# Performance work log

Measured on AMD Instinct MI355X. Metric: run time of the kernel, lower is better.

## Reference

```python
import jax, jax.numpy as jnp
import numpy as np

N, F, H, Z = 80, 64, 256, 128
OFF = N * (N - 1) // 2  # 3160
E = 800
MPM_ITERS = 50


def _gcn(x, src, dst, W, b, n):
    # PyG GCNConv: add self-loops, symmetric normalization D^-1/2 (A+I) D^-1/2, then +bias
    h = x @ W
    ones = jnp.ones(src.shape[0], dtype=h.dtype)
    deg = jax.ops.segment_sum(ones, dst, num_segments=n)
    dinv = jax.lax.rsqrt(jnp.maximum(deg, 1e-12))
    norm = dinv[src] * dinv[dst]
    out = jax.ops.segment_sum(h[src] * norm[:, None], dst, num_segments=n)
    return out + b


def _bn(h, g, b):
    # BatchNorm1d, training mode (biased batch stats), eps=1e-5
    m = h.mean(0)
    v = ((h - m) ** 2).mean(0)
    return g * (h - m) * jax.lax.rsqrt(v + 1e-5) + b


def setup_inputs() -> dict:
    key = jax.random.key(0)
    ks = jax.random.split(key, 32)
    rn = lambda k, s, sc=0.05: (jax.random.normal(k, s, dtype=jnp.float32) * sc)
    inp = {
        'x': jax.random.normal(ks[0], (N, F), dtype=jnp.float32),
        'edge_index': jax.random.randint(ks[1], (2, E), 0, N, dtype=jnp.int32),
        'adj': jax.random.randint(ks[2], (N, N), 0, 2, dtype=jnp.int32),
        'eps': jax.random.normal(ks[3], (1, Z), dtype=jnp.float32),
        'W1': rn(ks[4], (F, H)), 'b1': jnp.zeros((H,), jnp.float32),
        'g1': jnp.ones((H,), jnp.float32), 'bt1': jnp.zeros((H,), jnp.float32),
        'W2': rn(ks[5], (H, H)), 'b2': jnp.zeros((H,), jnp.float32),
        'g2': jnp.ones((H,), jnp.float32), 'bt2': jnp.zeros((H,), jnp.float32),
        'Wmu': rn(ks[6], (H, Z)), 'bmu': jnp.zeros((Z,), jnp.float32),
        'Wlv': rn(ks[7], (H, Z)), 'blv': jnp.zeros((Z,), jnp.float32),
        'We1': rn(ks[8], (Z, H)), 'be1': jnp.zeros((H,), jnp.float32),
        'We2': rn(ks[9], (H, OFF)), 'be2': jnp.zeros((OFF,), jnp.float32),
        'Wn1': rn(ks[10], (Z, H)), 'bn1': jnp.zeros((H,), jnp.float32),
        'Wn2': rn(ks[11], (H, N)), 'bn2': jnp.zeros((N,), jnp.float32),
    }
    return inp


def reference(x, edge_index, adj, eps, W1, b1, g1, bt1, W2, b2, g2, bt2,
              Wmu, bmu, Wlv, blv, We1, be1, We2, be2, Wn1, bn1, Wn2, bn2):
    n = N
    # ---- encoder: GCN -> BN -> ReLU (x2), mean pool over real nodes ----
    sl = jnp.arange(n, dtype=edge_index.dtype)
    src = jnp.concatenate([edge_index[0], sl])
    dst = jnp.concatenate([edge_index[1], sl])
    h = jax.nn.relu(_bn(_gcn(x, src, dst, W1, b1, n), g1, bt1))
    h = jax.nn.relu(_bn(_gcn(h, src, dst, W2, b2, n), g2, bt2))
    g_vec = h.sum(0, keepdims=True) / n  # [1,H], R_int == n
    mu = g_vec @ Wmu + bmu
    logvar = jnp.clip(g_vec @ Wlv + blv, -4.0, 4.0)
    z = mu + eps * jnp.exp(0.5 * logvar)  # reparam
    # ---- decoder ----
    vec_logits = (jax.nn.relu(z @ We1 + be1) @ We2 + be2)[0]   # [OFF]
    node_logits = (jax.nn.relu(z @ Wn1 + bn1) @ Wn2 + bn2)[0]  # [N]
    iu, ju = np.triu_indices(n, k=1)
    A_hat = jnp.zeros((n, n), jnp.float32).at[iu, ju].set(vec_logits)
    A_hat = A_hat + A_hat.T
    d = jnp.arange(n)
    A_hat = A_hat.at[d, d].set(node_logits)  # A_hat_logits
    # ---- edge similarity tensor S [N,N,N,N] ----
    A = jnp.maximum(adj, adj.T).astype(jnp.float32)
    A = A.at[d, d].set(1.0)
    B = jax.nn.sigmoid(A_hat).at[d, d].set(1.0)
    degA, degB = A.sum(1), B.sum(1)
    node_sim = 1.0 / (jnp.abs(degA[:, None] - degB[None, :]) + 1.0)
    dA, dB = jnp.diag(A), jnp.diag(B)  # all ones by construction (faithful to source)
    S = (A * dA[:, None] * dA[None, :])[:, :, None, None] * \
        (B * dB[:, None] * dB[None, :])[None, None, :, :]
    eye = jnp.eye(n, dtype=bool)
    xor = eye[:, :, None, None] ^ eye[None, None, :, :]
    S = jnp.where(xor, 0.0, S)
    both = eye[:, :, None, None] & eye[None, None, :, :]
    S = jnp.where(both, node_sim[:, None, :, None], S)
    # ---- MPM fixed point (fixed 50 iterations) ----
    notey = (~eye).astype(S.dtype)[:, :, None]  # [i,j,1]
    X0 = jnp.full((n, n), 1.0 / n, dtype=jnp.float32)

    def step(X, _):
        node_term = X * node_sim
        XS_max = jnp.max(S * X[None, :, None, :], axis=-1)  # [i,j,a] = max_b X[j,b]*S[i,j,a,b]
        edge_term = jnp.sum(XS_max * notey, axis=1)          # sum over j != i
        Xn = node_term + edge_term
        Xn = Xn / jnp.linalg.norm(Xn)
        return Xn, None

    X, _ = jax.lax.scan(step, X0, None, length=MPM_ITERS)
    return X
```

## Files before the change

### kernel.cpp

```cpp
#include <hip/hip_runtime.h>


#define NN 80
#define PBLK 20
#define TPB 320
#define RP 84
#define NCOLS 13

__device__ __forceinline__ float ld_f32g(const float* p){
  return __hip_atomic_load((float*)p, __ATOMIC_RELAXED, __HIP_MEMORY_SCOPE_AGENT);
}
__device__ __forceinline__ void st_f32g(float* p, float v){
  __hip_atomic_store(p, v, __ATOMIC_RELAXED, __HIP_MEMORY_SCOPE_AGENT);
}
__device__ __forceinline__ int ld_i32g(const int* p){
  return __hip_atomic_load((int*)p, __ATOMIC_RELAXED, __HIP_MEMORY_SCOPE_AGENT);
}
__device__ __forceinline__ void st_i32g(int* p, int v){
  __hip_atomic_store(p, v, __ATOMIC_RELAXED, __HIP_MEMORY_SCOPE_AGENT);
}
__device__ __forceinline__ float2 ld_f2g(const float* p){
  union { unsigned long long u; float2 f; } c;
  c.u = __hip_atomic_load((unsigned long long*)p, __ATOMIC_RELAXED, __HIP_MEMORY_SCOPE_AGENT);
  return c.f;
}
__device__ __forceinline__ void st_f2g(float* p, float a, float b){
  union { unsigned long long u; float2 f; } c; c.f.x = a; c.f.y = b;
  __hip_atomic_store((unsigned long long*)p, c.u, __ATOMIC_RELAXED, __HIP_MEMORY_SCOPE_AGENT);
}

__device__ __forceinline__ float wave_sum(float v){
  #pragma unroll
  for (int k = 32; k >= 1; k >>= 1) v += __shfl_xor(v, k, 64);
  return v;
}

__device__ void gcn_bn_relu(const float* inL, const float* bias, const float* gamma,
                            const float* beta, const int* ei, const float* dinvS,
                            float* accL, float* colstat, int p, int tid)
{
  for (int u = tid; u < NCOLS*NN; u += TPB) accL[u] = 0.f;
  __syncthreads();
  for (int cl = 0; cl < NCOLS; cl++){
    int c = p + PBLK*cl; if (c >= 256) break;
    const float* col = &inL[cl*NN];
    for (int e = tid; e < 800; e += TPB){
      int s = ei[e], d = ei[800+e];
      atomicAdd(&accL[cl*NN + d], col[s]*dinvS[s]*dinvS[d]);
    }
  }
  __syncthreads();
  for (int u = tid; u < NCOLS*NN; u += TPB){
    int cl = u/NN, i = u - cl*NN, c = p + PBLK*cl;
    if (c < 256) accL[u] += inL[u]*dinvS[i]*dinvS[i] + bias[c];
  }
  __syncthreads();
  if (tid < 16*NCOLS){
    int g = tid >> 4, s = tid & 15, c = p + PBLK*g;
    if (c < 256){
      float r[5];
      float sm = 0.f;
      #pragma unroll
      for (int i = 0; i < 5; i++){ r[i] = accL[g*NN + s + 16*i]; sm += r[i]; }
      #pragma unroll
      for (int k = 1; k < 16; k <<= 1) sm += __shfl_xor(sm, k, 64);
      float m = sm*(1.0f/NN);
      float sq = 0.f;
      #pragma unroll
      for (int i = 0; i < 5; i++){ float d = r[i]-m; sq += d*d; }
      #pragma unroll
      for (int k = 1; k < 16; k <<= 1) sq += __shfl_xor(sq, k, 64);
      if (s == 0){
        colstat[2*g]   = m;
        colstat[2*g+1] = 1.0f/sqrtf(sq*(1.0f/NN) + 1e-5f);
      }
    }
  }
  __syncthreads();
  for (int u = tid; u < NCOLS*NN; u += TPB){
    int cl = u/NN, c = p + PBLK*cl;
    if (c < 256){
      float hv = gamma[c]*(accL[u]-colstat[2*cl])*colstat[2*cl+1] + beta[c];
      accL[u] = fmaxf(hv, 0.f);
    }
  }
  __syncthreads();
}

__global__ __launch_bounds__(TPB, 1) void gvae_fused(
    const float* __restrict__ x,  const int* __restrict__ ei, const int* __restrict__ adj,
    const float* __restrict__ eps,
    const float* __restrict__ W1, const float* __restrict__ b1, const float* __restrict__ g1, const float* __restrict__ bt1,
    const float* __restrict__ W2, const float* __restrict__ b2, const float* __restrict__ g2, const float* __restrict__ bt2,
    const float* __restrict__ Wmu,const float* __restrict__ bmu,const float* __restrict__ Wlv,const float* __restrict__ blv,
    const float* __restrict__ We1,const float* __restrict__ be1,const float* __restrict__ We2,const float* __restrict__ be2,
    float* __restrict__ out, float* __restrict__ ws)
{
  const int tid = threadIdx.x;
  const int p   = blockIdx.x;

  int*   flag  = (int*)ws;
  float* slots = ws + 32;
  float* gvS   = ws + 1056;
  float* hT    = ws + 1312;
  float* Bm    = hT + 20480;
  float* Xb0   = Bm + 6400;
  float* Xb1   = Xb0 + 6400;

  __shared__ float Xs[NN*RP];
  __shared__ float MtL[4*RP];
  __shared__ float red[8];
  __shared__ float scS;
  __shared__ float dinvS[NN];
  __shared__ float accL[NCOLS*NN];
  __shared__ float hL[NCOLS*NN];
  __shared__ float gv[256], zv[128], t1v[256];
  __shared__ float colstat[2*NCOLS];

  for (int i = tid; i < NN; i += TPB) accL[i] = 1.0f;
  __syncthreads();
  for (int e = tid; e < 800; e += TPB) atomicAdd(&accL[ei[800+e]], 1.0f);
  __syncthreads();
  for (int i = tid; i < NN; i += TPB) dinvS[i] = 1.0f/sqrtf(accL[i]);
  __syncthreads();

  for (int u = tid; u < NCOLS*NN; u += TPB){
    int cl = u/NN, i = u - cl*NN, c = p + PBLK*cl;
    if (c < 256){
      float s = 0.f;
      for (int k = 0; k < 64; k++) s += x[i*64+k]*W1[k*256+c];
      hL[u] = s;
    }
  }
  __syncthreads();
  gcn_bn_relu(hL, b1, g1, bt1, ei, dinvS, accL, colstat, p, tid);
  for (int u2 = tid; u2 < 40*NCOLS; u2 += TPB){
    int cl = u2/40, i2 = (u2 - cl*40)*2, c = p + PBLK*cl;
    if (c < 256) st_f2g(&hT[c*NN+i2], accL[cl*NN+i2], accL[cl*NN+i2+1]);
  }
  __syncthreads();
  if (tid == 0) st_i32g(&flag[p], 1);

  if (tid < PBLK) while (ld_i32g(&flag[tid]) < 1) {}
  __syncthreads();
  for (int u = tid; u < 20*NCOLS; u += TPB){
    int cl = u/20, iq = u - cl*20, c = p + PBLK*cl;
    if (c < 256){
      int i0 = 4*iq;
      float a0=0.f,a1=0.f,a2=0.f,a3=0.f;
      for (int k = 0; k < 256; k++){
        float wv = W2[k*256+c];
        float2 h01 = ld_f2g(&hT[k*NN+i0]);
        float2 h23 = ld_f2g(&hT[k*NN+i0+2]);
        a0 += h01.x*wv; a1 += h01.y*wv; a2 += h23.x*wv; a3 += h23.y*wv;
      }
      hL[cl*NN+i0+0]=a0; hL[cl*NN+i0+1]=a1; hL[cl*NN+i0+2]=a2; hL[cl*NN+i0+3]=a3;
    }
  }
  __syncthreads();
  gcn_bn_relu(hL, b2, g2, bt2, ei, dinvS, accL, colstat, p, tid);
  if (tid < 16*NCOLS){
    int g = tid >> 4, s = tid & 15, c = p + PBLK*g;
    if (c < 256){
      float sm = 0.f;
      #pragma unroll
      for (int i = 0; i < 5; i++) sm += accL[g*NN + s + 16*i];
      #pragma unroll
      for (int k = 1; k < 16; k <<= 1) sm += __shfl_xor(sm, k, 64);
      if (s == 0) st_f32g(&gvS[c], sm*(1.0f/NN));
    }
  }
  __syncthreads();
  if (tid == 0) st_i32g(&flag[p], 2);

  if (tid < PBLK) while (ld_i32g(&flag[tid]) < 2) {}
  __syncthreads();
  if (tid < 256) gv[tid] = ld_f32g(&gvS[tid]);
  __syncthreads();
  if (tid < 128){
    int c = tid;
    float smu = bmu[c], slv = blv[c];
    for (int k = 0; k < 256; k++){
      float g = gv[k];
      smu += g*Wmu[k*128+c];
      slv += g*Wlv[k*128+c];
    }
    slv = fminf(fmaxf(slv, -4.f), 4.f);
    zv[c] = smu + eps[c]*expf(0.5f*slv);
  }
  __syncthreads();
  if (tid < 256){
    float s = be1[tid];
    for (int k = 0; k < 128; k++) s += zv[k]*We1[k*256+tid];
    t1v[tid] = fmaxf(s, 0.f);
  }
  __syncthreads();

  {
    int c0 = 79-p, c1 = 59-p, c2 = 39-p, c3 = 19-p;
    int t1b = c0+c1, t2b = t1b+c2, L = t2b+c3;
    int i = -1, j = -1;
    if      (tid < c0) { i = p;    j = p+1 +tid;        }
    else if (tid < t1b){ i = p+20; j = p+21+(tid-c0);   }
    else if (tid < t2b){ i = p+40; j = p+41+(tid-t1b);  }
    else if (tid < L)  { i = p+60; j = p+61+(tid-t2b);  }
    if (i >= 0){
      int off = i*(159-i)/2 + (j-i-1);
      float s = be2[off];
      for (int k = 0; k < 256; k++) s += t1v[k]*We2[k*3160+off];
      float sg = 1.0f/(1.0f + expf(-s));
      st_f32g(&Bm[i*NN+j], sg);
      st_f32g(&Bm[j*NN+i], sg);
    }
    if (tid >= 316){
      int r = tid-316, ii = p+20*r;
      st_f32g(&Bm[ii*NN+ii], 1.0f);
    }
  }
  __syncthreads();
  if (tid == 0) st_i32g(&flag[p], 3);

  const int w  = tid >> 6;
  const int l  = tid & 63;
  const int il = 16*w + (l & 15);
  const int ae = l >> 4;
  const int al = 4*p + ae;

  float4 Af[20];
  float degA = 0.f;
  #pragma unroll
  for (int c = 0; c < 20; c++){
    int j0 = 4*c;
    int4 ar = *(const int4*)&adj[il*NN+j0];
    int q0 = adj[(j0+0)*NN+il];
    int q1 = adj[(j0+1)*NN+il];
    int q2 = adj[(j0+2)*NN+il];
    int q3 = adj[(j0+3)*NN+il];
    float4 a;
    a.x = ((ar.x|q0) != 0 || il == j0+0) ? 1.f : 0.f;
    a.y = ((ar.y|q1) != 0 || il == j0+1) ? 1.f : 0.f;
    a.z = ((ar.z|q2) != 0 || il == j0+2) ? 1.f : 0.f;
    a.w = ((ar.w|q3) != 0 || il == j0+3) ? 1.f : 0.f;
    Af[c] = a;
    degA += (a.x+a.y)+(a.z+a.w);
  }

  if (tid < PBLK) while (ld_i32g(&flag[tid]) < 3) {}
  __syncthreads();

  float4 Bf[20];
  float degB = 0.f;
  #pragma unroll
  for (int c = 0; c < 20; c++){
    float2 b01 = ld_f2g(&Bm[al*NN+4*c]);
    float2 b23 = ld_f2g(&Bm[al*NN+4*c+2]);
    Bf[c].x = b01.x; Bf[c].y = b01.y; Bf[c].z = b23.x; Bf[c].w = b23.y;
    degB += (b01.x+b01.y)+(b23.x+b23.y);
  }
  const float ns = 1.0f/(fabsf(degA-degB)+1.0f);
  {
    if      (ae == 0) Bf[p].x = 0.f;
    else if (ae == 1) Bf[p].y = 0.f;
    else if (ae == 2) Bf[p].z = 0.f;
    else              Bf[p].w = 0.f;
  }

  for (int u = tid; u < NN*RP; u += TPB) Xs[u] = 1.0f/NN;
  __syncthreads();
  float xn = 0.f;
  for (int t = 0; t < 50; t++){
    float sc = 1.0f;
    if (t > 0){
      float pv = 0.f;
      if (tid < PBLK){
        const float* sp = &slots[(t-1)*PBLK + tid];
        do { pv = ld_f32g(sp); } while (pv == 0.0f);
      }
      if (w == 0){
        float v = pv;
        #pragma unroll
        for (int k = 1; k < 32; k <<= 1) v += __shfl_xor(v, k, 64);
        if (tid == 0) scS = 1.0f/sqrtf(v);
      }
      __syncthreads();
      sc = scS;
      const float* Xsrc = ((t-1)&1) ? Xb1 : Xb0;
      #pragma unroll
      for (int q = 0; q < 10; q++){
        int p2 = tid + TPB*q;
        int j = p2/40, c2 = p2 - 40*j;
        float2 xv = ld_f2g(&Xsrc[j*NN + 2*c2]);
        Xs[j*RP + 2*c2]     = xv.x;
        Xs[j*RP + 2*c2 + 1] = xv.y;
      }
      __syncthreads();
    }

    float m = 0.f;
    #pragma unroll
    for (int c = 0; c < 20; c++){
      float4 xv = *(const float4*)&Xs[il*RP+4*c];
      float p0 = xv.x*Bf[c].x, p1 = xv.y*Bf[c].y, p2 = xv.z*Bf[c].z, p3 = xv.w*Bf[c].w;
      m = fmaxf(m, fmaxf(fmaxf(p0,p1), fmaxf(p2,p3)));
    }
    float xnode = Xs[il*RP+al];
    MtL[ae*RP+il] = m;
    __syncthreads();

    float e0=0.f,e1=0.f,e2=0.f,e3=0.f;
    #pragma unroll
    for (int c = 0; c < 20; c++){
      float4 mv = *(const float4*)&MtL[ae*RP+4*c];
      e0 += Af[c].x*mv.x; e1 += Af[c].y*mv.y; e2 += Af[c].z*mv.z; e3 += Af[c].w*mv.w;
    }
    float edge = ((e0+e1)+(e2+e3)) - m;
    xn = sc*(ns*xnode + edge);

    if (t < 49){
      float* Xdst = (t&1) ? Xb1 : Xb0;
      st_f32g(&Xdst[il*NN+al], xn);
    }
    float v2 = wave_sum(xn*xn);
    if (l == 0) red[w] = v2;
    __syncthreads();
    if (tid == 0){
      float tot = ((red[0]+red[1])+(red[2]+red[3]))+red[4];
      st_f32g(&slots[t*PBLK+p], tot);
    }
  }

  {
    float pv = 0.f;
    if (tid < PBLK){
      const float* sp = &slots[49*PBLK + tid];
      do { pv = ld_f32g(sp); } while (pv == 0.0f);
    }
    if (w == 0){
      float v = pv;
      #pragma unroll
      for (int k = 1; k < 32; k <<= 1) v += __shfl_xor(v, k, 64);
      if (tid == 0) scS = 1.0f/sqrtf(v);
    }
    __syncthreads();
    out[il*NN+al] = xn * scS;
  }
}

extern "C" void kernel_launch(void* const* d_in, const int* in_sizes, int n_in,
                              void* d_out, int out_size, void* d_ws, size_t ws_size,
                              hipStream_t stream)
{
  (void)in_sizes; (void)n_in; (void)out_size; (void)ws_size;
  hipMemsetAsync(d_ws, 0, 4224, stream);
  gvae_fused<<<PBLK, TPB, 0, stream>>>(
      (const float*)d_in[0],  (const int*)d_in[1],   (const int*)d_in[2],   (const float*)d_in[3],
      (const float*)d_in[4],  (const float*)d_in[5],  (const float*)d_in[6],  (const float*)d_in[7],
      (const float*)d_in[8],  (const float*)d_in[9],  (const float*)d_in[10], (const float*)d_in[11],
      (const float*)d_in[12], (const float*)d_in[13], (const float*)d_in[14], (const float*)d_in[15],
      (const float*)d_in[16], (const float*)d_in[17], (const float*)d_in[18], (const float*)d_in[19],
      (float*)d_out, (float*)d_ws);
}
```

Measured before the change: 568.9 us.

## Compute decoder B rows locally, stage hT in LDS, coalesce X exchange stores

Each block now computes the four rows of the decoded sigmoid matrix it needs directly into shared memory. This removes the global Bm buffer and the grid-wide flag-3 barrier, at the cost of computing each off-diagonal entry twice across blocks. The second GCN matmul stages hT into LDS in 64-row chunks instead of reading global memory per thread. The MPM iteration stages outputs in LDS so they can be written as contiguous float2 per block, and the read side transposes into Xs. That adds one extra __syncthreads per iteration.

New measurement: 612.0 us. 7.6% more time.

```diff
diff --git a/kernel.cpp b/kernel.cpp
--- a/kernel.cpp
+++ b/kernel.cpp
@@ -5,6 +5,7 @@
 #define PBLK 20
 #define TPB 320
 #define RP 84
+#define RPB 84
 #define NCOLS 13
 
 __device__ __forceinline__ float ld_f32g(const float* p){
@@ -103,12 +104,13 @@
   float* slots = ws + 32;
   float* gvS   = ws + 1056;
   float* hT    = ws + 1312;
-  float* Bm    = hT + 20480;
-  float* Xb0   = Bm + 6400;
+  float* Xb0   = hT + 20480;
   float* Xb1   = Xb0 + 6400;
 
-  __shared__ float Xs[NN*RP];
+  __shared__ float poolS[NN*RP];
   __shared__ float MtL[4*RP];
+  __shared__ float xnT[4*NN];
+  __shared__ float BmL[4*RPB];
   __shared__ float red[8];
   __shared__ float scS;
   __shared__ float dinvS[NN];
@@ -116,6 +118,7 @@
   __shared__ float hL[NCOLS*NN];
   __shared__ float gv[256], zv[128], t1v[256];
   __shared__ float colstat[2*NCOLS];
+  float* Xs = poolS;
 
   for (int i = tid; i < NN; i += TPB) accL[i] = 1.0f;
   __syncthreads();
@@ -143,17 +146,31 @@
 
   if (tid < PBLK) while (ld_i32g(&flag[tid]) < 1) {}
   __syncthreads();
-  for (int u = tid; u < 20*NCOLS; u += TPB){
-    int cl = u/20, iq = u - cl*20, c = p + PBLK*cl;
-    if (c < 256){
-      int i0 = 4*iq;
-      float a0=0.f,a1=0.f,a2=0.f,a3=0.f;
-      for (int k = 0; k < 256; k++){
-        float wv = W2[k*256+c];
-        float2 h01 = ld_f2g(&hT[k*NN+i0]);
-        float2 h23 = ld_f2g(&hT[k*NN+i0+2]);
-        a0 += h01.x*wv; a1 += h01.y*wv; a2 += h23.x*wv; a3 += h23.y*wv;
-      }
+  {
+    const int cl = tid/20, iq = tid - 20*cl, c = p + PBLK*cl;
+    const int i0 = 4*iq;
+    const bool valid = (tid < 20*NCOLS) && (c < 256);
+    float a0=0.f, a1=0.f, a2=0.f, a3=0.f;
+    for (int ch = 0; ch < 4; ch++){
+      const int k0 = 64*ch;
+      __syncthreads();
+      #pragma unroll
+      for (int r = 0; r < 8; r++){
+        int u = tid + TPB*r;
+        float2 hv = ld_f2g(&hT[k0*NN + 2*u]);
+        poolS[2*u] = hv.x; poolS[2*u+1] = hv.y;
+      }
+      __syncthreads();
+      if (valid){
+        for (int kk = 0; kk < 64; kk++){
+          float wv = W2[(k0+kk)*256 + c];
+          float4 hv = *(const float4*)&poolS[kk*NN + i0];
+          a0 += hv.x*wv; a1 += hv.y*wv; a2 += hv.z*wv; a3 += hv.w*wv;
+        }
+      }
+    }
+    __syncthreads();
+    if (valid){
       hL[cl*NN+i0+0]=a0; hL[cl*NN+i0+1]=a1; hL[cl*NN+i0+2]=a2; hL[cl*NN+i0+3]=a3;
     }
   }
@@ -196,29 +213,20 @@
   }
   __syncthreads();
 
-  {
-    int c0 = 79-p, c1 = 59-p, c2 = 39-p, c3 = 19-p;
-    int t1b = c0+c1, t2b = t1b+c2, L = t2b+c3;
-    int i = -1, j = -1;
-    if      (tid < c0) { i = p;    j = p+1 +tid;        }
-    else if (tid < t1b){ i = p+20; j = p+21+(tid-c0);   }
-    else if (tid < t2b){ i = p+40; j = p+41+(tid-t1b);  }
-    else if (tid < L)  { i = p+60; j = p+61+(tid-t2b);  }
-    if (i >= 0){
-      int off = i*(159-i)/2 + (j-i-1);
-      float s = be2[off];
-      for (int k = 0; k < 256; k++) s += t1v[k]*We2[k*3160+off];
-      float sg = 1.0f/(1.0f + expf(-s));
-      st_f32g(&Bm[i*NN+j], sg);
-      st_f32g(&Bm[j*NN+i], sg);
-    }
-    if (tid >= 316){
-      int r = tid-316, ii = p+20*r;
-      st_f32g(&Bm[ii*NN+ii], 1.0f);
-    }
-  }
-  __syncthreads();
-  if (tid == 0) st_i32g(&flag[p], 3);
+  if (tid < 316){
+    int r = tid/79, jj = tid - 79*r;
+    int a = 4*p + r;
+    int j = jj + (jj >= a ? 1 : 0);
+    int lo = a < j ? a : j, hi = a < j ? j : a;
+    int off = lo*(159-lo)/2 + (hi-lo-1);
+    float s = be2[off];
+    for (int k = 0; k < 256; k++) s += t1v[k]*We2[k*3160+off];
+    BmL[r*RPB + j] = 1.0f/(1.0f + expf(-s));
+  } else {
+    int r = tid-316;
+    BmL[r*RPB + 4*p + r] = 1.0f;
+  }
+  __syncthreads();
 
   const int w  = tid >> 6;
   const int l  = tid & 63;
@@ -245,17 +253,13 @@
     degA += (a.x+a.y)+(a.z+a.w);
   }
 
-  if (tid < PBLK) while (ld_i32g(&flag[tid]) < 3) {}
-  __syncthreads();
-
   float4 Bf[20];
   float degB = 0.f;
   #pragma unroll
   for (int c = 0; c < 20; c++){
-    float2 b01 = ld_f2g(&Bm[al*NN+4*c]);
-    float2 b23 = ld_f2g(&Bm[al*NN+4*c+2]);
-    Bf[c].x = b01.x; Bf[c].y = b01.y; Bf[c].z = b23.x; Bf[c].w = b23.y;
-    degB += (b01.x+b01.y)+(b23.x+b23.y);
+    float4 b = *(const float4*)&BmL[ae*RPB + 4*c];
+    Bf[c] = b;
+    degB += (b.x+b.y)+(b.z+b.w);
   }
   const float ns = 1.0f/(fabsf(degA-degB)+1.0f);
   {
@@ -264,6 +268,7 @@
     else if (ae == 2) Bf[p].z = 0.f;
     else              Bf[p].w = 0.f;
   }
+  __syncthreads();
 
   for (int u = tid; u < NN*RP; u += TPB) Xs[u] = 1.0f/NN;
   __syncthreads();
@@ -287,11 +292,11 @@
       const float* Xsrc = ((t-1)&1) ? Xb1 : Xb0;
       #pragma unroll
       for (int q = 0; q < 10; q++){
-        int p2 = tid + TPB*q;
-        int j = p2/40, c2 = p2 - 40*j;
-        float2 xv = ld_f2g(&Xsrc[j*NN + 2*c2]);
-        Xs[j*RP + 2*c2]     = xv.x;
-        Xs[j*RP + 2*c2 + 1] = xv.y;
+        int u = tid + TPB*q;
+        int a = u/40, j2 = (u - 40*a)*2;
+        float2 xv = ld_f2g(&Xsrc[a*NN + j2]);
+        Xs[j2*RP + a]     = xv.x;
+        Xs[(j2+1)*RP + a] = xv.y;
       }
       __syncthreads();
     }
@@ -316,12 +321,14 @@
     float edge = ((e0+e1)+(e2+e3)) - m;
     xn = sc*(ns*xnode + edge);
 
-    if (t < 49){
-      float* Xdst = (t&1) ? Xb1 : Xb0;
-      st_f32g(&Xdst[il*NN+al], xn);
-    }
+    if (t < 49) xnT[ae*NN + il] = xn;
     float v2 = wave_sum(xn*xn);
     if (l == 0) red[w] = v2;
+    __syncthreads();
+    if (t < 49 && tid < 160){
+      float* Xdst = (t&1) ? Xb1 : Xb0;
+      st_f2g(&Xdst[p*320 + 2*tid], xnT[2*tid], xnT[2*tid+1]);
+    }
     __syncthreads();
     if (tid == 0){
       float tot = ((red[0]+red[1])+(red[2]+red[3]))+red[4];
```
